# Kernel tuning notes

Hardware: AMD Instinct MI355X
Metric: run time of the kernel (lower is better)

## Reference

```python
import jax, jax.numpy as jnp
import numpy as np

D_MODEL = 128
N_HEADS = 4
HEAD_DIM = D_MODEL // N_HEADS


def setup_inputs() -> dict:
    key = jax.random.key(0)
    ks = jax.random.split(key, 16)
    s = 0.05
    B, N, T = 1, 1024, 1024
    return {
        "node_states": jax.random.normal(ks[0], (B, N, D_MODEL), jnp.float32),
        "task_features": jax.random.normal(ks[1], (T, D_MODEL), jnp.float32),
        "in_proj_w": jax.random.normal(ks[2], (3 * D_MODEL, D_MODEL), jnp.float32) * s,
        "in_proj_b": jnp.zeros((3 * D_MODEL,), jnp.float32),
        "out_w": jax.random.normal(ks[3], (D_MODEL, D_MODEL), jnp.float32) * s,
        "out_b": jnp.zeros((D_MODEL,), jnp.float32),
        "W1": jax.random.normal(ks[4], (256, 256), jnp.float32) * s,
        "b1": jnp.zeros((256,), jnp.float32),
        "W2": jax.random.normal(ks[5], (128, 256), jnp.float32) * s,
        "b2": jnp.zeros((128,), jnp.float32),
        "W3": jax.random.normal(ks[6], (1, 128), jnp.float32) * s,
        "b3": jnp.zeros((1,), jnp.float32),
        "Wc1": jax.random.normal(ks[7], (256, D_MODEL), jnp.float32) * s,
        "bc1": jnp.zeros((256,), jnp.float32),
        "Wc2": jax.random.normal(ks[8], (32, 256), jnp.float32) * s,
        "bc2": jnp.zeros((32,), jnp.float32),
    }


def _mha(x, in_proj_w, in_proj_b, out_w, out_b):
    # x: [B, N, D]; torch nn.MultiheadAttention self-attention, batch_first.
    B, N, D = x.shape
    q = x @ in_proj_w[:D].T + in_proj_b[:D]
    k = x @ in_proj_w[D:2 * D].T + in_proj_b[D:2 * D]
    v = x @ in_proj_w[2 * D:].T + in_proj_b[2 * D:]
    def split(t):  # [B,N,D] -> [B,H,N,dh]
        return t.reshape(B, N, N_HEADS, HEAD_DIM).transpose(0, 2, 1, 3)
    qh, kh, vh = split(q), split(k), split(v)
    scores = jnp.einsum("bhqd,bhkd->bhqk", qh, kh) / jnp.sqrt(jnp.float32(HEAD_DIM))
    attn = jax.nn.softmax(scores, axis=-1)  # [B,H,N,N]
    ctx = jnp.einsum("bhqk,bhkd->bhqd", attn, vh)
    ctx = ctx.transpose(0, 2, 1, 3).reshape(B, N, D)
    out = ctx @ out_w.T + out_b
    attn_avg = attn.mean(axis=1)  # torch averages heads by default -> [B,N,N]
    return out, attn_avg


def reference(node_states, task_features, in_proj_w, in_proj_b, out_w, out_b,
              W1, b1, W2, b2, W3, b3, Wc1, bc1, Wc2, bc2):
    attended, attn_w = _mha(node_states, in_proj_w, in_proj_b, out_w, out_b)
    nodes = attended[0]  # original loop only uses batch 0: [N, D]
    # Linear on concat([task, node]) == split-weight sum; vectorize pairwise.
    t1 = task_features @ W1[:, :D_MODEL].T          # [T, 256]
    n1 = nodes @ W1[:, D_MODEL:].T                  # [N, 256]
    h1 = jax.nn.relu(t1[:, None, :] + n1[None, :, :] + b1)      # [T, N, 256]
    h2 = jax.nn.relu(jnp.einsum("tnc,kc->tnk", h1, W2) + b2)   # [T, N, 128]
    matching_scores = jax.nn.sigmoid(jnp.einsum("tnk,ok->tn", h2, W3) + b3[0])
    global_state = attended.mean(axis=1)            # [B, D]
    coordination_logits = jax.nn.relu(global_state @ Wc1.T + bc1) @ Wc2.T + bc2
    return matching_scores, coordination_logits, attn_w
```

## Files before the change

kernel.cpp:

```cpp
#include <hip/hip_runtime.h>
#include <hip/hip_fp16.h>
#include <stdint.h>


typedef __attribute__((ext_vector_type(4))) float floatx4;
typedef __attribute__((ext_vector_type(8))) _Float16 half8;

#define OFF_QKV  0x000000u
#define OFF_T1H  0x280000u
#define OFF_N1H  0x300000u
#define OFF_W2F  0x380000u
#define OFF_GS   0x398000u
#define OFF_SC   0x400000u

__device__ __forceinline__ unsigned pkadd(unsigned a, unsigned b) {
    unsigned r; asm("v_pk_add_f16 %0, %1, %2" : "=v"(r) : "v"(a), "v"(b)); return r;
}
__device__ __forceinline__ unsigned pkmax(unsigned a, unsigned b) {
    unsigned r; asm("v_pk_max_f16 %0, %1, %2" : "=v"(r) : "v"(a), "v"(b)); return r;
}
__device__ __forceinline__ unsigned pk2h(float a, float b) {
    return (unsigned)__half_as_ushort(__float2half(a)) |
           ((unsigned)__half_as_ushort(__float2half(b)) << 16);
}

template<bool BIAS, bool F16OUT>
__device__ __forceinline__ void gemm_dev(
    const float* __restrict__ A, int lda,
    const float* __restrict__ B, int ldb,
    const float* __restrict__ bias,
    void* __restrict__ Cv, int ldc, int K, float scale,
    int m0, int n0, float (*As)[64], float (*Bs)[64])
{
    const int tid = threadIdx.x;
    const int tx = tid & 15, ty = tid >> 4;
    const int lr = tid >> 2;
    const int lk = (tid & 3) * 4;
    float c[4][4] = {};

    for (int k0 = 0; k0 < K; k0 += 16) {
        float4 a  = *(const float4*)&A[(long)(m0 + lr) * lda + k0 + lk];
        float4 bb = *(const float4*)&B[(long)(n0 + lr) * ldb + k0 + lk];
        __syncthreads();
        As[lk + 0][lr] = a.x;  As[lk + 1][lr] = a.y;  As[lk + 2][lr] = a.z;  As[lk + 3][lr] = a.w;
        Bs[lk + 0][lr] = bb.x; Bs[lk + 1][lr] = bb.y; Bs[lk + 2][lr] = bb.z; Bs[lk + 3][lr] = bb.w;
        __syncthreads();
#pragma unroll
        for (int k = 0; k < 16; k++) {
            float4 av = *(const float4*)&As[k][ty * 4];
            float4 bv = *(const float4*)&Bs[k][tx * 4];
            c[0][0] += av.x * bv.x; c[0][1] += av.x * bv.y; c[0][2] += av.x * bv.z; c[0][3] += av.x * bv.w;
            c[1][0] += av.y * bv.x; c[1][1] += av.y * bv.y; c[1][2] += av.y * bv.z; c[1][3] += av.y * bv.w;
            c[2][0] += av.z * bv.x; c[2][1] += av.z * bv.y; c[2][2] += av.z * bv.z; c[2][3] += av.z * bv.w;
            c[3][0] += av.w * bv.x; c[3][1] += av.w * bv.y; c[3][2] += av.w * bv.z; c[3][3] += av.w * bv.w;
        }
    }

    float bsv[4] = {0.f, 0.f, 0.f, 0.f};
    if (BIAS) {
        float4 t = *(const float4*)&bias[n0 + tx * 4];
        bsv[0] = t.x; bsv[1] = t.y; bsv[2] = t.z; bsv[3] = t.w;
    }
#pragma unroll
    for (int i = 0; i < 4; i++) {
        float v0 = c[i][0] * scale + bsv[0];
        float v1 = c[i][1] * scale + bsv[1];
        float v2 = c[i][2] * scale + bsv[2];
        float v3 = c[i][3] * scale + bsv[3];
        long m = m0 + ty * 4 + i;
        if (F16OUT) {
            unsigned short* Cp = (unsigned short*)Cv;
            ushort4 o;
            o.x = __half_as_ushort(__float2half(v0));
            o.y = __half_as_ushort(__float2half(v1));
            o.z = __half_as_ushort(__float2half(v2));
            o.w = __half_as_ushort(__float2half(v3));
            *(ushort4*)&Cp[m * ldc + n0 + tx * 4] = o;
        } else {
            float* Cp = (float*)Cv;
            *(float4*)&Cp[m * ldc + n0 + tx * 4] = make_float4(v0, v1, v2, v3);
        }
    }
}

__launch_bounds__(256)
__global__ void proj_fused(const float* __restrict__ node, const float* __restrict__ ipw,
                           const float* __restrict__ ipb,
                           const float* __restrict__ task, const float* __restrict__ W1,
                           const float* __restrict__ b1, const float* __restrict__ W2,
                           float* __restrict__ qkv, unsigned short* __restrict__ t1h,
                           unsigned short* __restrict__ w2f)
{
    __shared__ float As[16][64], Bs[16][64];
    const int bid = blockIdx.x;
    if (bid < 96) {
        gemm_dev<true, false>(node, 128, ipw, 128, ipb, qkv, 384, 128, 1.0f,
                              (bid & 15) * 64, (bid >> 4) * 64, As, Bs);
    } else if (bid < 160) {
        const int b = bid - 96;
        gemm_dev<true, true>(task, 128, W1, 256, b1, t1h, 256, 128, 1.0f,
                             (b & 15) * 64, (b >> 4) * 64, As, Bs);
    } else {
        const int gtid = (bid - 160) * 256 + threadIdx.x;
        const int lane = gtid & 63, frag = gtid >> 6;
        const int cc = frag >> 3, ot = frag & 7;
        const float* src = &W2[(ot * 16 + (lane & 15)) * 256 + cc * 32 + (lane >> 4) * 8];
        uint4 o;
        o.x = pk2h(src[0], src[1]);
        o.y = pk2h(src[2], src[3]);
        o.z = pk2h(src[4], src[5]);
        o.w = pk2h(src[6], src[7]);
        ((uint4*)w2f)[gtid] = o;
    }
}

__launch_bounds__(256)
__global__ void scores_kernel(const float* __restrict__ qkv, float* __restrict__ sc)
{
    __shared__ float As[16][64], Bs[16][64];
    const int h = blockIdx.z;
    gemm_dev<false, false>(qkv + h * 32, 384, qkv + 128 + h * 32, 384, nullptr,
                           sc + (long)h * 1048576, 1024, 32, 0.17677669529663687f,
                           blockIdx.x * 64, blockIdx.y * 64, As, Bs);
}

__launch_bounds__(256)
__global__ void attn_mega(const float* __restrict__ sc, const float* __restrict__ qkv,
                          const float* __restrict__ outw, const float* __restrict__ outb,
                          const float* __restrict__ W1,
                          float* __restrict__ attn_out, unsigned short* __restrict__ n1h,
                          float* __restrict__ gs)
{
    __shared__ unsigned short Ps[16 * 1024];
    __shared__ float ctp[2][4][128];
    __shared__ float attr[4][128];
    __shared__ float stm[16], stl[16];
    const int t = threadIdx.x;
    const int q0 = blockIdx.x * 4;

#pragma unroll
    for (int r = 0; r < 16; r++) {
        const int h = r >> 2, q = r & 3;
        float4 v = *(const float4*)&sc[(long)h * 1048576 + (long)(q0 + q) * 1024 + t * 4];
        ushort4 o;
        o.x = __half_as_ushort(__float2half(v.x));
        o.y = __half_as_ushort(__float2half(v.y));
        o.z = __half_as_ushort(__float2half(v.z));
        o.w = __half_as_ushort(__float2half(v.w));
        *(ushort4*)&Ps[r * 1024 + t * 4] = o;
    }
    __syncthreads();

    {
        const int h = t >> 6, ln = t & 63;
#pragma unroll
        for (int q = 0; q < 4; q++) {
            const int base = (h * 4 + q) * 1024 + ln * 16;
            float v[16];
            float mx = -1e30f;
#pragma unroll
            for (int i = 0; i < 8; i++) {
                float2 f = __half22float2(*(const __half2*)&Ps[base + i * 2]);
                v[2 * i] = f.x; v[2 * i + 1] = f.y;
                mx = fmaxf(mx, fmaxf(f.x, f.y));
            }
#pragma unroll
            for (int m = 1; m < 64; m <<= 1) mx = fmaxf(mx, __shfl_xor(mx, m));
            float s = 0.f;
#pragma unroll
            for (int i = 0; i < 16; i++) s += __expf(v[i] - mx);
#pragma unroll
            for (int m = 1; m < 64; m <<= 1) s += __shfl_xor(s, m);
            if (ln == 0) { stm[h * 4 + q] = mx; stl[h * 4 + q] = s; }
        }
    }
    __syncthreads();

    {
        float acc[4][4] = {};
#pragma unroll
        for (int r = 0; r < 16; r++) {
            const int q = r & 3;
            const float m = stm[r], il = 1.0f / stl[r];
            ushort4 u = *(const ushort4*)&Ps[r * 1024 + t * 4];
            float p0 = __expf(__half2float(__ushort_as_half(u.x)) - m) * il;
            float p1 = __expf(__half2float(__ushort_as_half(u.y)) - m) * il;
            float p2 = __expf(__half2float(__ushort_as_half(u.z)) - m) * il;
            float p3 = __expf(__half2float(__ushort_as_half(u.w)) - m) * il;
            ushort4 o;
            o.x = __half_as_ushort(__float2half(p0));
            o.y = __half_as_ushort(__float2half(p1));
            o.z = __half_as_ushort(__float2half(p2));
            o.w = __half_as_ushort(__float2half(p3));
            *(ushort4*)&Ps[r * 1024 + t * 4] = o;
            acc[q][0] += 0.25f * p0; acc[q][1] += 0.25f * p1;
            acc[q][2] += 0.25f * p2; acc[q][3] += 0.25f * p3;
        }
#pragma unroll
        for (int q = 0; q < 4; q++)
            *(float4*)&attn_out[(long)(q0 + q) * 1024 + t * 4] =
                make_float4(acc[q][0], acc[q][1], acc[q][2], acc[q][3]);
    }
    __syncthreads();

    {
        const int hd = t & 127, ks = t >> 7;
        const int h = hd >> 5;
        float ca[4] = {};
        const float* vp = qkv + 256 + hd;
        for (int k0 = ks * 512; k0 < ks * 512 + 512; k0 += 4) {
            float v0 = vp[(long)(k0 + 0) * 384];
            float v1 = vp[(long)(k0 + 1) * 384];
            float v2 = vp[(long)(k0 + 2) * 384];
            float v3 = vp[(long)(k0 + 3) * 384];
#pragma unroll
            for (int q = 0; q < 4; q++) {
                float2 fa = __half22float2(*(const __half2*)&Ps[(h * 4 + q) * 1024 + k0]);
                float2 fb = __half22float2(*(const __half2*)&Ps[(h * 4 + q) * 1024 + k0 + 2]);
                ca[q] += fa.x * v0 + fa.y * v1 + fb.x * v2 + fb.y * v3;
            }
        }
#pragma unroll
        for (int q = 0; q < 4; q++) ctp[ks][q][hd] = ca[q];
    }
    __syncthreads();
    {
        float* cf = &ctp[0][0][0];
        cf[t] += cf[t + 512];
        cf[t + 256] += cf[t + 768];
    }
    __syncthreads();

    {
        const int j = t & 127, qp = t >> 7;
        float a0 = outb[j], a1 = a0;
        const float* wr = &outw[j * 128];
        for (int d = 0; d < 128; d += 4) {
            float4 w  = *(const float4*)&wr[d];
            float4 c0 = *(const float4*)&ctp[0][qp * 2 + 0][d];
            float4 c1 = *(const float4*)&ctp[0][qp * 2 + 1][d];
            a0 += w.x * c0.x + w.y * c0.y + w.z * c0.z + w.w * c0.w;
            a1 += w.x * c1.x + w.y * c1.y + w.z * c1.z + w.w * c1.w;
        }
        attr[qp * 2 + 0][j] = a0;
        attr[qp * 2 + 1][j] = a1;
    }
    __syncthreads();
    if (t < 128) atomicAdd(&gs[t], attr[0][t] + attr[1][t] + attr[2][t] + attr[3][t]);

    {
        const int c = t;
        const float* wr = &W1[c * 256 + 128];
        float n[4] = {};
        for (int d = 0; d < 128; d += 4) {
            float4 w = *(const float4*)&wr[d];
#pragma unroll
            for (int q = 0; q < 4; q++) {
                float4 a = *(const float4*)&attr[q][d];
                n[q] += w.x * a.x + w.y * a.y + w.z * a.z + w.w * a.w;
            }
        }
#pragma unroll
        for (int q = 0; q < 4; q++)
            n1h[(long)(q0 + q) * 256 + c] = __half_as_ushort(__float2half(n[q]));
    }
}

__launch_bounds__(256, 2)
__global__ void score_kernel(const unsigned short* __restrict__ t1h,
                             const unsigned short* __restrict__ n1h,
                             const unsigned short* __restrict__ w2f,
                             const float* __restrict__ b2, const float* __restrict__ W3,
                             const float* __restrict__ b3, float* __restrict__ out,
                             const float* __restrict__ gs,
                             const float* __restrict__ Wc1, const float* __restrict__ bc1,
                             const float* __restrict__ Wc2, const float* __restrict__ bc2,
                             float* __restrict__ outc)
{
    __shared__ unsigned short w2s[32768];
    const int tid = threadIdx.x;

    if (blockIdx.y == 32) {
        if (blockIdx.x != 0) return;
        float* g  = (float*)w2s;
        float* hh = g + 128;
        if (tid < 128) g[tid] = gs[tid] * (1.0f / 1024.0f);
        __syncthreads();
        {
            float a = bc1[tid];
            const float* wr = &Wc1[tid * 128];
            for (int d = 0; d < 128; d += 4) {
                float4 w = *(const float4*)&wr[d];
                a += w.x * g[d] + w.y * g[d + 1] + w.z * g[d + 2] + w.w * g[d + 3];
            }
            hh[tid] = fmaxf(a, 0.f);
        }
        __syncthreads();
        if (tid < 32) {
            float a = bc2[tid];
            const float* wr = &Wc2[tid * 256];
            for (int c = 0; c < 256; c += 4) {
                float4 w = *(const float4*)&wr[c];
                a += w.x * hh[c] + w.y * hh[c + 1] + w.z * hh[c + 2] + w.w * hh[c + 3];
            }
            outc[tid] = a;
        }
        return;
    }

    const int lane = tid & 63;
    const int wv = tid >> 6;
    const int col = lane & 15;
    const int quad = lane >> 4;
    const int nb = blockIdx.x * 64 + wv * 16;
    const int tb = blockIdx.y * 32;

    {
        const uint4* src = (const uint4*)w2f;
        uint4* dst = (uint4*)w2s;
#pragma unroll
        for (int i = 0; i < 16; i++) dst[tid + i * 256] = src[tid + i * 256];
    }

    const int myn = nb + col;
    uint4 n1p[8];
#pragma unroll
    for (int cc = 0; cc < 8; cc++)
        n1p[cc] = *(const uint4*)(n1h + (long)myn * 256 + cc * 32 + quad * 8);

    const float b3s = b3[0];
    __syncthreads();

    for (int tg = 0; tg < 8; tg++) {
        floatx4 acc[4][8];
#pragma unroll
        for (int ot = 0; ot < 8; ot++) {
            float4 bq = *(const float4*)&b2[ot * 16 + quad * 4];
            floatx4 ini; ini[0] = bq.x; ini[1] = bq.y; ini[2] = bq.z; ini[3] = bq.w;
#pragma unroll
            for (int tt = 0; tt < 4; tt++) acc[tt][ot] = ini;
        }

#pragma unroll
        for (int cc = 0; cc < 8; cc++) {
            uint4 tp[4];
#pragma unroll
            for (int tt = 0; tt < 4; tt++)
                tp[tt] = *(const uint4*)(t1h + (long)(tb + tg * 4 + tt) * 256 + cc * 32 + quad * 8);

            const unsigned* npu = (const unsigned*)&n1p[cc];
            union { unsigned u[4]; half8 h; } af[4];
#pragma unroll
            for (int tt = 0; tt < 4; tt++) {
                const unsigned* tpu = (const unsigned*)&tp[tt];
#pragma unroll
                for (int p = 0; p < 4; p++)
                    af[tt].u[p] = pkmax(pkadd(tpu[p], npu[p]), 0u);
            }
#pragma unroll
            for (int ot = 0; ot < 8; ot++) {
                union { uint4 u; half8 h; } bf;
                bf.u = *(const uint4*)&w2s[((cc * 8 + ot) * 64 + lane) * 8];
#pragma unroll
                for (int tt = 0; tt < 4; tt++)
                    acc[tt][ot] = __builtin_amdgcn_mfma_f32_16x16x32_f16(bf.h, af[tt].h, acc[tt][ot], 0, 0, 0);
            }
        }

        float outv = 0.f;
#pragma unroll
        for (int tt = 0; tt < 4; tt++) {
            float pa = 0.f, pb = 0.f;
#pragma unroll
            for (int ot = 0; ot < 8; ot++) {
                float4 wq = *(const float4*)&W3[ot * 16 + quad * 4];
                floatx4 a = acc[tt][ot];
                pa += fmaxf(a[0], 0.f) * wq.x + fmaxf(a[2], 0.f) * wq.z;
                pb += fmaxf(a[1], 0.f) * wq.y + fmaxf(a[3], 0.f) * wq.w;
            }
            float p = pa + pb;
            p += __shfl_xor(p, 16);
            p += __shfl_xor(p, 32);
            if (quad == tt) outv = p;
        }
        out[(long)(tb + tg * 4 + quad) * 1024 + nb + col] =
            1.0f / (1.0f + __expf(-(outv + b3s)));
    }
}

extern "C" void kernel_launch(void* const* d_in, const int* in_sizes, int n_in,
                              void* d_out, int out_size, void* d_ws, size_t ws_size,
                              hipStream_t stream)
{
    const float* node = (const float*)d_in[0];
    const float* task = (const float*)d_in[1];
    const float* ipw  = (const float*)d_in[2];
    const float* ipb  = (const float*)d_in[3];
    const float* outw = (const float*)d_in[4];
    const float* outb = (const float*)d_in[5];
    const float* W1   = (const float*)d_in[6];
    const float* b1   = (const float*)d_in[7];
    const float* W2   = (const float*)d_in[8];
    const float* b2   = (const float*)d_in[9];
    const float* W3   = (const float*)d_in[10];
    const float* b3   = (const float*)d_in[11];
    const float* Wc1  = (const float*)d_in[12];
    const float* bc1  = (const float*)d_in[13];
    const float* Wc2  = (const float*)d_in[14];
    const float* bc2  = (const float*)d_in[15];

    char* ws = (char*)d_ws;
    float* qkv = (float*)(ws + OFF_QKV);
    float* sc  = (float*)(ws + OFF_SC);
    unsigned short* t1h = (unsigned short*)(ws + OFF_T1H);
    unsigned short* n1h = (unsigned short*)(ws + OFF_N1H);
    unsigned short* w2f = (unsigned short*)(ws + OFF_W2F);
    float* gs = (float*)(ws + OFF_GS);

    float* out_match = (float*)d_out;
    float* out_coord = out_match + 1048576;
    float* out_attn  = out_coord + 32;

    hipMemsetAsync(gs, 0, 512, stream);
    proj_fused<<<dim3(176, 1, 1), 256, 0, stream>>>(
        node, ipw, ipb, task, W1, b1, W2, qkv, t1h, w2f);
    scores_kernel<<<dim3(16, 16, 4), 256, 0, stream>>>(qkv, sc);
    attn_mega<<<dim3(256, 1, 1), 256, 0, stream>>>(
        sc, qkv, outw, outb, W1, out_attn, n1h, gs);
    score_kernel<<<dim3(16, 33, 1), 256, 0, stream>>>(
        t1h, n1h, w2f, b2, W3, b3, out_match,
        gs, Wc1, bc1, Wc2, bc2, out_coord);
}
```

Measured before the change: 235.3 us.

## Fuse QK score GEMM into attention kernel with MFMA, drop scores buffer

Removes the separate scores_kernel and its 16 MB fp32 score buffer. attn_mega now computes Q·K^T directly with f16 MFMA per block, writing the scaled scores into shared memory as fp16. The gs memset moves into an extra block of proj_fused, and score_kernel caches b2/W3 in shared memory and prefetches W2 fragments one step ahead. This cuts a kernel launch and a large global write and reread, at the cost of every attention block recomputing K conversions and reading all of K from global memory.

```diff
diff --git a/kernel.cpp b/kernel.cpp
--- a/kernel.cpp
+++ b/kernel.cpp
@@ -11,7 +11,6 @@
 #define OFF_N1H  0x300000u
 #define OFF_W2F  0x380000u
 #define OFF_GS   0x398000u
-#define OFF_SC   0x400000u
 
 __device__ __forceinline__ unsigned pkadd(unsigned a, unsigned b) {
     unsigned r; asm("v_pk_add_f16 %0, %1, %2" : "=v"(r) : "v"(a), "v"(b)); return r;
@@ -89,7 +88,7 @@
                            const float* __restrict__ task, const float* __restrict__ W1,
                            const float* __restrict__ b1, const float* __restrict__ W2,
                            float* __restrict__ qkv, unsigned short* __restrict__ t1h,
-                           unsigned short* __restrict__ w2f)
+                           unsigned short* __restrict__ w2f, float* __restrict__ gs)
 {
     __shared__ float As[16][64], Bs[16][64];
     const int bid = blockIdx.x;
@@ -100,7 +99,7 @@
         const int b = bid - 96;
         gemm_dev<true, true>(task, 128, W1, 256, b1, t1h, 256, 128, 1.0f,
                              (b & 15) * 64, (b >> 4) * 64, As, Bs);
-    } else {
+    } else if (bid < 176) {
         const int gtid = (bid - 160) * 256 + threadIdx.x;
         const int lane = gtid & 63, frag = gtid >> 6;
         const int cc = frag >> 3, ot = frag & 7;
@@ -111,21 +110,13 @@
         o.z = pk2h(src[4], src[5]);
         o.w = pk2h(src[6], src[7]);
         ((uint4*)w2f)[gtid] = o;
+    } else {
+        if (threadIdx.x < 128) gs[threadIdx.x] = 0.f;
     }
 }
 
 __launch_bounds__(256)
-__global__ void scores_kernel(const float* __restrict__ qkv, float* __restrict__ sc)
-{
-    __shared__ float As[16][64], Bs[16][64];
-    const int h = blockIdx.z;
-    gemm_dev<false, false>(qkv + h * 32, 384, qkv + 128 + h * 32, 384, nullptr,
-                           sc + (long)h * 1048576, 1024, 32, 0.17677669529663687f,
-                           blockIdx.x * 64, blockIdx.y * 64, As, Bs);
-}
-
-__launch_bounds__(256)
-__global__ void attn_mega(const float* __restrict__ sc, const float* __restrict__ qkv,
+__global__ void attn_mega(const float* __restrict__ qkv,
                           const float* __restrict__ outw, const float* __restrict__ outb,
                           const float* __restrict__ W1,
                           float* __restrict__ attn_out, unsigned short* __restrict__ n1h,
@@ -136,18 +127,43 @@
     __shared__ float attr[4][128];
     __shared__ float stm[16], stl[16];
     const int t = threadIdx.x;
+    const int lane = t & 63, wv = t >> 6;
+    const int li = lane & 15, quad = lane >> 4;
     const int q0 = blockIdx.x * 4;
 
-#pragma unroll
-    for (int r = 0; r < 16; r++) {
-        const int h = r >> 2, q = r & 3;
-        float4 v = *(const float4*)&sc[(long)h * 1048576 + (long)(q0 + q) * 1024 + t * 4];
-        ushort4 o;
-        o.x = __half_as_ushort(__float2half(v.x));
-        o.y = __half_as_ushort(__float2half(v.y));
-        o.z = __half_as_ushort(__float2half(v.z));
-        o.w = __half_as_ushort(__float2half(v.w));
-        *(ushort4*)&Ps[r * 1024 + t * 4] = o;
+    {
+        const int h_ = li >> 2, q_ = li & 3;
+        const float scl = 0.17677669529663687f;
+        const float* qrow = qkv + (long)(q0 + q_) * 384 + h_ * 32 + quad * 8;
+        float4 qa = *(const float4*)qrow;
+        float4 qb = *(const float4*)(qrow + 4);
+        union { unsigned u[4]; half8 h; } aq;
+        aq.u[0] = pk2h(qa.x * scl, qa.y * scl);
+        aq.u[1] = pk2h(qa.z * scl, qa.w * scl);
+        aq.u[2] = pk2h(qb.x * scl, qb.y * scl);
+        aq.u[3] = pk2h(qb.z * scl, qb.w * scl);
+        for (int ch = 0; ch < 16; ch++) {
+            const int kt = wv * 256 + ch * 16;
+            const float* kb0 = qkv + (long)(kt + li) * 384 + 128 + quad * 8;
+#pragma unroll
+            for (int h = 0; h < 4; h++) {
+                float4 ka = *(const float4*)(kb0 + h * 32);
+                float4 kbv = *(const float4*)(kb0 + h * 32 + 4);
+                union { unsigned u[4]; half8 h8; } bk;
+                bk.u[0] = pk2h(ka.x, ka.y);
+                bk.u[1] = pk2h(ka.z, ka.w);
+                bk.u[2] = pk2h(kbv.x, kbv.y);
+                bk.u[3] = pk2h(kbv.z, kbv.w);
+                floatx4 d = {0.f, 0.f, 0.f, 0.f};
+                d = __builtin_amdgcn_mfma_f32_16x16x32_f16(aq.h, bk.h8, d, 0, 0, 0);
+                if (quad == h) {
+#pragma unroll
+                    for (int r = 0; r < 4; r++)
+                        Ps[(h * 4 + r) * 1024 + kt + li] =
+                            __half_as_ushort(__float2half(d[r]));
+                }
+            }
+        }
     }
     __syncthreads();
 
@@ -278,6 +294,7 @@
                              float* __restrict__ outc)
 {
     __shared__ unsigned short w2s[32768];
+    __shared__ float b2s[128], w3s[128];
     const int tid = threadIdx.x;
 
     if (blockIdx.y == 32) {
@@ -320,6 +337,7 @@
         uint4* dst = (uint4*)w2s;
 #pragma unroll
         for (int i = 0; i < 16; i++) dst[tid + i * 256] = src[tid + i * 256];
+        if (tid < 128) { b2s[tid] = b2[tid]; w3s[tid] = W3[tid]; }
     }
 
     const int myn = nb + col;
@@ -335,12 +353,13 @@
         floatx4 acc[4][8];
 #pragma unroll
         for (int ot = 0; ot < 8; ot++) {
-            float4 bq = *(const float4*)&b2[ot * 16 + quad * 4];
+            float4 bq = *(const float4*)&b2s[ot * 16 + quad * 4];
             floatx4 ini; ini[0] = bq.x; ini[1] = bq.y; ini[2] = bq.z; ini[3] = bq.w;
 #pragma unroll
             for (int tt = 0; tt < 4; tt++) acc[tt][ot] = ini;
         }
 
+        uint4 bfc = *(const uint4*)&w2s[(size_t)lane * 8];
 #pragma unroll
         for (int cc = 0; cc < 8; cc++) {
             uint4 tp[4];
@@ -359,24 +378,33 @@
             }
 #pragma unroll
             for (int ot = 0; ot < 8; ot++) {
-                union { uint4 u; half8 h; } bf;
-                bf.u = *(const uint4*)&w2s[((cc * 8 + ot) * 64 + lane) * 8];
+                const int nf = cc * 8 + ot + 1;
+                uint4 bfn;
+                if (nf < 64) bfn = *(const uint4*)&w2s[((size_t)nf * 64 + lane) * 8];
+                union { uint4 u; half8 h; } bf; bf.u = bfc;
 #pragma unroll
                 for (int tt = 0; tt < 4; tt++)
                     acc[tt][ot] = __builtin_amdgcn_mfma_f32_16x16x32_f16(bf.h, af[tt].h, acc[tt][ot], 0, 0, 0);
-            }
-        }
-
+                bfc = bfn;
+            }
+        }
+
+        floatx4 w3r[8];
+#pragma unroll
+        for (int ot = 0; ot < 8; ot++) {
+            float4 wq = *(const float4*)&w3s[ot * 16 + quad * 4];
+            w3r[ot][0] = wq.x; w3r[ot][1] = wq.y; w3r[ot][2] = wq.z; w3r[ot][3] = wq.w;
+        }
         float outv = 0.f;
 #pragma unroll
         for (int tt = 0; tt < 4; tt++) {
             float pa = 0.f, pb = 0.f;
 #pragma unroll
             for (int ot = 0; ot < 8; ot++) {
-                float4 wq = *(const float4*)&W3[ot * 16 + quad * 4];
                 floatx4 a = acc[tt][ot];
-                pa += fmaxf(a[0], 0.f) * wq.x + fmaxf(a[2], 0.f) * wq.z;
-                pb += fmaxf(a[1], 0.f) * wq.y + fmaxf(a[3], 0.f) * wq.w;
+                floatx4 w = w3r[ot];
+                pa += fmaxf(a[0], 0.f) * w[0] + fmaxf(a[2], 0.f) * w[2];
+                pb += fmaxf(a[1], 0.f) * w[1] + fmaxf(a[3], 0.f) * w[3];
             }
             float p = pa + pb;
             p += __shfl_xor(p, 16);
@@ -411,7 +439,6 @@
 
     char* ws = (char*)d_ws;
     float* qkv = (float*)(ws + OFF_QKV);
-    float* sc  = (float*)(ws + OFF_SC);
     unsigned short* t1h = (unsigned short*)(ws + OFF_T1H);
     unsigned short* n1h = (unsigned short*)(ws + OFF_N1H);
     unsigned short* w2f = (unsigned short*)(ws + OFF_W2F);
@@ -421,12 +448,10 @@
     float* out_coord = out_match + 1048576;
     float* out_attn  = out_coord + 32;
 
-    hipMemsetAsync(gs, 0, 512, stream);
-    proj_fused<<<dim3(176, 1, 1), 256, 0, stream>>>(
-        node, ipw, ipb, task, W1, b1, W2, qkv, t1h, w2f);
-    scores_kernel<<<dim3(16, 16, 4), 256, 0, stream>>>(qkv, sc);
+    proj_fused<<<dim3(177, 1, 1), 256, 0, stream>>>(
+        node, ipw, ipb, task, W1, b1, W2, qkv, t1h, w2f, gs);
     attn_mega<<<dim3(256, 1, 1), 256, 0, stream>>>(
-        sc, qkv, outw, outb, W1, out_attn, n1h, gs);
+        qkv, outw, outb, W1, out_attn, n1h, gs);
     score_kernel<<<dim3(16, 33, 1), 256, 0, stream>>>(
         t1h, n1h, w2f, b2, W3, b3, out_match,
         gs, Wc1, bc1, Wc2, bc2, out_coord);
```

New measurement: 252.6 us. +7.4%, slower.

## Stage task tile in LDS, split W2 between LDS and global, fold memset

Applied to the files above, without the earlier changes.

The score kernel now stages its 32-row task-feature tile (t1h) in shared memory instead of re-reading it from global for every t-group. To make room, only the first 5 of 8 W2 fragment chunks stay in LDS and the rest are read from global/L2 inside the MFMA loop. Bias b2 and W3 are moved to LDS and b2 is added in the epilogue instead of pre-initialising the accumulators. The hipMemsetAsync of gs is folded into an extra block of proj_fused to save a launch. The global W2 reads in the inner loop may add latency, traded against lower LDS use and possibly better occupancy.

```diff
diff --git a/kernel.cpp b/kernel.cpp
--- a/kernel.cpp
+++ b/kernel.cpp
@@ -89,7 +89,7 @@
                            const float* __restrict__ task, const float* __restrict__ W1,
                            const float* __restrict__ b1, const float* __restrict__ W2,
                            float* __restrict__ qkv, unsigned short* __restrict__ t1h,
-                           unsigned short* __restrict__ w2f)
+                           unsigned short* __restrict__ w2f, float* __restrict__ gs)
 {
     __shared__ float As[16][64], Bs[16][64];
     const int bid = blockIdx.x;
@@ -100,7 +100,7 @@
         const int b = bid - 96;
         gemm_dev<true, true>(task, 128, W1, 256, b1, t1h, 256, 128, 1.0f,
                              (b & 15) * 64, (b >> 4) * 64, As, Bs);
-    } else {
+    } else if (bid < 176) {
         const int gtid = (bid - 160) * 256 + threadIdx.x;
         const int lane = gtid & 63, frag = gtid >> 6;
         const int cc = frag >> 3, ot = frag & 7;
@@ -111,6 +111,8 @@
         o.z = pk2h(src[4], src[5]);
         o.w = pk2h(src[6], src[7]);
         ((uint4*)w2f)[gtid] = o;
+    } else {
+        if (threadIdx.x < 128) gs[threadIdx.x] = 0.f;
     }
 }
 
@@ -277,12 +279,14 @@
                              const float* __restrict__ Wc2, const float* __restrict__ bc2,
                              float* __restrict__ outc)
 {
-    __shared__ unsigned short w2s[32768];
+    __shared__ unsigned short w2s[20480];
+    __shared__ unsigned short t1s[8192];
+    __shared__ float b2s[128], w3s[128];
     const int tid = threadIdx.x;
 
     if (blockIdx.y == 32) {
         if (blockIdx.x != 0) return;
-        float* g  = (float*)w2s;
+        float* g  = (float*)t1s;
         float* hh = g + 128;
         if (tid < 128) g[tid] = gs[tid] * (1.0f / 1024.0f);
         __syncthreads();
@@ -319,7 +323,14 @@
         const uint4* src = (const uint4*)w2f;
         uint4* dst = (uint4*)w2s;
 #pragma unroll
-        for (int i = 0; i < 16; i++) dst[tid + i * 256] = src[tid + i * 256];
+        for (int i = 0; i < 10; i++) dst[tid + i * 256] = src[tid + i * 256];
+        uint4* t1dst = (uint4*)t1s;
+#pragma unroll
+        for (int i = 0; i < 8; i++) {
+            const int j = tid + i * 256;
+            t1dst[j] = *(const uint4*)(t1h + (long)(tb + (j >> 5)) * 256 + (j & 31) * 8);
+        }
+        if (tid < 128) { b2s[tid] = b2[tid]; w3s[tid] = W3[tid]; }
     }
 
     const int myn = nb + col;
@@ -332,21 +343,14 @@
     __syncthreads();
 
     for (int tg = 0; tg < 8; tg++) {
-        floatx4 acc[4][8];
-#pragma unroll
-        for (int ot = 0; ot < 8; ot++) {
-            float4 bq = *(const float4*)&b2[ot * 16 + quad * 4];
-            floatx4 ini; ini[0] = bq.x; ini[1] = bq.y; ini[2] = bq.z; ini[3] = bq.w;
-#pragma unroll
-            for (int tt = 0; tt < 4; tt++) acc[tt][ot] = ini;
-        }
+        floatx4 acc[4][8] = {};
 
 #pragma unroll
         for (int cc = 0; cc < 8; cc++) {
             uint4 tp[4];
 #pragma unroll
             for (int tt = 0; tt < 4; tt++)
-                tp[tt] = *(const uint4*)(t1h + (long)(tb + tg * 4 + tt) * 256 + cc * 32 + quad * 8);
+                tp[tt] = *(const uint4*)&t1s[(tg * 4 + tt) * 256 + cc * 32 + quad * 8];
 
             const unsigned* npu = (const unsigned*)&n1p[cc];
             union { unsigned u[4]; half8 h; } af[4];
@@ -360,25 +364,32 @@
 #pragma unroll
             for (int ot = 0; ot < 8; ot++) {
                 union { uint4 u; half8 h; } bf;
-                bf.u = *(const uint4*)&w2s[((cc * 8 + ot) * 64 + lane) * 8];
+                if (cc < 5)
+                    bf.u = *(const uint4*)&w2s[((cc * 8 + ot) * 64 + lane) * 8];
+                else
+                    bf.u = *(const uint4*)(w2f + ((size_t)((cc * 8 + ot) * 64 + lane)) * 8);
 #pragma unroll
                 for (int tt = 0; tt < 4; tt++)
                     acc[tt][ot] = __builtin_amdgcn_mfma_f32_16x16x32_f16(bf.h, af[tt].h, acc[tt][ot], 0, 0, 0);
             }
         }
 
+        float part[4] = {0.f, 0.f, 0.f, 0.f};
+#pragma unroll
+        for (int ot = 0; ot < 8; ot++) {
+            float4 bq = *(const float4*)&b2s[ot * 16 + quad * 4];
+            float4 wq = *(const float4*)&w3s[ot * 16 + quad * 4];
+#pragma unroll
+            for (int tt = 0; tt < 4; tt++) {
+                floatx4 a = acc[tt][ot];
+                part[tt] += fmaxf(a[0] + bq.x, 0.f) * wq.x + fmaxf(a[1] + bq.y, 0.f) * wq.y
+                          + fmaxf(a[2] + bq.z, 0.f) * wq.z + fmaxf(a[3] + bq.w, 0.f) * wq.w;
+            }
+        }
         float outv = 0.f;
 #pragma unroll
         for (int tt = 0; tt < 4; tt++) {
-            float pa = 0.f, pb = 0.f;
-#pragma unroll
-            for (int ot = 0; ot < 8; ot++) {
-                float4 wq = *(const float4*)&W3[ot * 16 + quad * 4];
-                floatx4 a = acc[tt][ot];
-                pa += fmaxf(a[0], 0.f) * wq.x + fmaxf(a[2], 0.f) * wq.z;
-                pb += fmaxf(a[1], 0.f) * wq.y + fmaxf(a[3], 0.f) * wq.w;
-            }
-            float p = pa + pb;
+            float p = part[tt];
             p += __shfl_xor(p, 16);
             p += __shfl_xor(p, 32);
             if (quad == tt) outv = p;
@@ -421,9 +432,8 @@
     float* out_coord = out_match + 1048576;
     float* out_attn  = out_coord + 32;
 
-    hipMemsetAsync(gs, 0, 512, stream);
-    proj_fused<<<dim3(176, 1, 1), 256, 0, stream>>>(
-        node, ipw, ipb, task, W1, b1, W2, qkv, t1h, w2f);
+    proj_fused<<<dim3(177, 1, 1), 256, 0, stream>>>(
+        node, ipw, ipb, task, W1, b1, W2, qkv, t1h, w2f, gs);
     scores_kernel<<<dim3(16, 16, 4), 256, 0, stream>>>(qkv, sc);
     attn_mega<<<dim3(256, 1, 1), 256, 0, stream>>>(
         sc, qkv, outw, outb, W1, out_attn, n1h, gs);
```

Result: slower. 274.8 us (+16.8%).
